# Kernel tuning notes

Measured on AMD Instinct MI355X. Metric: run time of the kernel, lower is better.

Reference implementation:

```python
import jax, jax.numpy as jnp
import numpy as np

TEMPERATURE = 0.1
LOSS_WEIGHT = 1.0


def setup_inputs() -> dict:
    key = jax.random.key(0)
    k1, k2 = jax.random.split(key)
    B, M, N, C = 8, 4096, 4096, 3
    pred_points = jax.random.normal(k1, (B, M, C), dtype=jnp.float32)
    gt_points = jax.random.normal(k2, (B, N, C), dtype=jnp.float32)
    return {"pred_points": pred_points, "gt_points": gt_points}


def _cdist(x, y):
    # Euclidean distance matrix [B, M, N] via the |x|^2 + |y|^2 - 2<x,y> identity
    x2 = jnp.sum(x * x, axis=-1)  # [B, M]
    y2 = jnp.sum(y * y, axis=-1)  # [B, N]
    xy = jnp.einsum('bmc,bnc->bmn', x, y)  # [B, M, N]
    d2 = x2[:, :, None] + y2[:, None, :] - 2.0 * xy
    return jnp.sqrt(jnp.maximum(d2, 0.0))


def reference(pred_points, gt_points):
    dists = _cdist(pred_points, gt_points)                # [B, M, N]
    soft_assign = jax.nn.softmax(-dists / TEMPERATURE, axis=2)  # softmin
    weighted = jnp.sum(soft_assign * dists, axis=2)       # [B, M]
    per_batch = jnp.mean(weighted, axis=1)                # [B]
    return jnp.mean(per_batch) * LOSS_WEIGHT              # scalar ('mean' reduction)
```

## Files before the change

### kernel.cpp

```cpp
#include <hip/hip_runtime.h>
#include <hip/hip_bf16.h>

#ifndef __has_builtin
#define __has_builtin(x) 0
#endif

#if __has_builtin(__builtin_amdgcn_exp2f)
#define FAST_EXP2(x) __builtin_amdgcn_exp2f(x)
#else
#define FAST_EXP2(x) exp2f(x)
#endif

#if __has_builtin(__builtin_amdgcn_sqrtf)
#define FAST_SQRT(x) __builtin_amdgcn_sqrtf(x)
#else
#define FAST_SQRT(x) sqrtf(x)
#endif

constexpr int kB = 8;
constexpr int kM = 4096;
constexpr int kN = 4096;
constexpr float C2  = 14.426950408889634f;
constexpr float C22 = C2 * C2;
#define POISON_U32 0xAAAAAAAAu

constexpr int RPL    = 4;
constexpr int ROWS   = 64 * RPL;
constexpr int WAVES  = 16;
constexpr int BLOCKT = 64 * WAVES;
constexpr int NROWG  = (kB * kM) / ROWS;
constexpr int    PART_OFF = 16;
constexpr size_t ws_need(int ns) { return (size_t)(PART_OFF + 2 * ns * kB * kM) * 4; }

template <int NSPLIT>
__global__ __launch_bounds__(BLOCKT, 8) void emd_partial_kernel(
    const float* __restrict__ pred, const float* __restrict__ gt,
    float* __restrict__ partL, float* __restrict__ partA) {
  constexpr int SEGN = kN / NSPLIT;
  constexpr int NPC  = SEGN / WAVES;
  __shared__ __align__(16) float4 g4[SEGN];
  __shared__ float red_l[WAVES][RPL][64];
  __shared__ float red_a[WAVES][RPL][64];

  const int tid  = threadIdx.x;
  const int lane = tid & 63;
  const int wv   = tid >> 6;
  const int rg   = blockIdx.x / NSPLIT;
  const int seg  = blockIdx.x % NSPLIT;
  const int rbase = rg * ROWS;
  const int b     = rbase >> 12;

  const float* gtb = gt + ((size_t)b * kN + (size_t)seg * SEGN) * 3;
  for (int i = tid; i < SEGN; i += BLOCKT) {
    const float* p = gtb + 3 * i;
    float x = p[0], y = p[1], z = p[2];
    g4[i] = make_float4(x, y, z, C22 * fmaf(x, x, fmaf(y, y, z * z)));
  }
  float nx[RPL], ny[RPL], nz[RPL], pq[RPL];
  const int m0 = (rbase & (kM - 1)) + lane;
#pragma unroll
  for (int r = 0; r < RPL; ++r) {
    const float* pp = pred + ((size_t)b * kM + m0 + r * 64) * 3;
    float x = pp[0], y = pp[1], z = pp[2];
    nx[r] = -2.0f * C22 * x;
    ny[r] = -2.0f * C22 * y;
    nz[r] = -2.0f * C22 * z;
    pq[r] = C22 * fmaf(x, x, fmaf(y, y, z * z));
  }
  __syncthreads();

  float l[RPL] = {};
  float a[RPL] = {};
  const int n0 = wv * NPC;
  for (int n = n0; n < n0 + NPC; n += 4) {
    float4 G[4];
#pragma unroll
    for (int j = 0; j < 4; ++j) G[j] = g4[n + j];
#pragma unroll
    for (int j = 0; j < 4; ++j) {
#pragma unroll
      for (int r = 0; r < RPL; ++r) {
        float s  = fmaf(nx[r], G[j].x,
                   fmaf(ny[r], G[j].y, fmaf(nz[r], G[j].z, G[j].w + pq[r])));
        float ds = FAST_SQRT(fmaxf(s, 0.0f));
        float p  = FAST_EXP2(-ds);
        l[r] += p;
        a[r] = fmaf(ds, p, a[r]);
      }
    }
  }
#pragma unroll
  for (int r = 0; r < RPL; ++r) {
    red_l[wv][r][lane] = l[r];
    red_a[wv][r][lane] = a[r];
  }
  __syncthreads();

  if (tid < 64 * RPL) {
    const int ln = tid & 63, r = tid >> 6;
    float lt = 0.f, at = 0.f;
#pragma unroll
    for (int c = 0; c < WAVES; ++c) { lt += red_l[c][r][ln]; at += red_a[c][r][ln]; }
    const int row = rbase + r * 64 + ln;
    partL[(size_t)seg * (kB * kM) + row] = lt;
    partA[(size_t)seg * (kB * kM) + row] = at;
  }
}

constexpr int CB      = 512;
constexpr int CBLOCKS = (kB * kM) / CB;
template <int NSEG>
__global__ __launch_bounds__(CB) void emd_combine_kernel(
    const float* __restrict__ partL, const float* __restrict__ partA,
    float* __restrict__ ws, float* __restrict__ out) {
  const int row = blockIdx.x * CB + threadIdx.x;
  float lt = 0.f, at = 0.f;
#pragma unroll
  for (int s = 0; s < NSEG; ++s) {
    lt += partL[(size_t)s * (kB * kM) + row];
    at += partA[(size_t)s * (kB * kM) + row];
  }
  float w = (at / lt) * (1.0f / (C2 * (float)(kB * kM)));
#pragma unroll
  for (int off = 32; off > 0; off >>= 1) w += __shfl_down(w, off, 64);
  __shared__ float sred[CB / 64];
  const int lane = threadIdx.x & 63, wv = threadIdx.x >> 6;
  if (lane == 0) sred[wv] = w;
  __syncthreads();
  if (threadIdx.x == 0) {
    float s = 0.f;
#pragma unroll
    for (int i = 0; i < CB / 64; ++i) s += sred[i];
    atomicAdd(&ws[0], s);
    __threadfence();
    unsigned t = atomicAdd((unsigned int*)(ws + 1), 1u);
    if (t == POISON_U32 + (unsigned)(CBLOCKS - 1)) {
      __threadfence();
      out[0] = atomicAdd(&ws[0], 0.0f);
    }
  }
}

constexpr int F_CHUNKS  = 16;
constexpr int F_BLOCKT  = 64 * F_CHUNKS;
constexpr int F_NPC     = kN / F_CHUNKS;
constexpr int F_NBLOCKS = (kB * kM) / 64;

__global__ __launch_bounds__(F_BLOCKT, 8) void emd_softmin_fallback(
    const float* __restrict__ pred, const float* __restrict__ gt,
    float* __restrict__ ws, float* __restrict__ out) {
  __shared__ __align__(16) float4 g4[kN];
  __shared__ float red_l[F_CHUNKS][64];
  __shared__ float red_a[F_CHUNKS][64];
  const int tid = threadIdx.x, lane = tid & 63, chunk = tid >> 6;
  const int rbase = blockIdx.x * 64;
  const int b = rbase >> 12;
  const int m = (rbase & (kM - 1)) + lane;
  const float* gtb = gt + (size_t)b * kN * 3;
  for (int i = tid; i < kN; i += F_BLOCKT) {
    const float* p = gtb + 3 * i;
    float x = p[0], y = p[1], z = p[2];
    g4[i] = make_float4(x, y, z, C22 * fmaf(x, x, fmaf(y, y, z * z)));
  }
  const float* pp_ptr = pred + ((size_t)b * kM + (size_t)m) * 3;
  const float px = pp_ptr[0], py = pp_ptr[1], pz = pp_ptr[2];
  const float nx = -2.0f * C22 * px, ny = -2.0f * C22 * py, nz = -2.0f * C22 * pz;
  const float pq = C22 * fmaf(px, px, fmaf(py, py, pz * pz));
  __syncthreads();
  float l0 = 0.f, l1 = 0.f, a0 = 0.f, a1 = 0.f;
  const int n0 = chunk * F_NPC;
#pragma unroll 2
  for (int n = n0; n < n0 + F_NPC; n += 2) {
    const float4 G0 = g4[n], G1 = g4[n + 1];
    {
      float s = fmaf(nx, G0.x, fmaf(ny, G0.y, fmaf(nz, G0.z, G0.w + pq)));
      float ds = FAST_SQRT(fmaxf(s, 0.f));
      float p = FAST_EXP2(-ds);
      l0 += p; a0 = fmaf(ds, p, a0);
    }
    {
      float s = fmaf(nx, G1.x, fmaf(ny, G1.y, fmaf(nz, G1.z, G1.w + pq)));
      float ds = FAST_SQRT(fmaxf(s, 0.f));
      float p = FAST_EXP2(-ds);
      l1 += p; a1 = fmaf(ds, p, a1);
    }
  }
  red_l[chunk][lane] = l0 + l1;
  red_a[chunk][lane] = a0 + a1;
  __syncthreads();
  if (tid < 64) {
    float lt = 0.f, at = 0.f;
#pragma unroll
    for (int c = 0; c < F_CHUNKS; ++c) { lt += red_l[c][tid]; at += red_a[c][tid]; }
    float w = (at / lt) * (1.0f / (C2 * (float)(kB * kM)));
#pragma unroll
    for (int off = 32; off > 0; off >>= 1) w += __shfl_down(w, off, 64);
    if (tid == 0) {
      atomicAdd(&ws[0], w);
      __threadfence();
      unsigned t = atomicAdd((unsigned int*)(ws + 1), 1u);
      if (t == POISON_U32 + (unsigned)(F_NBLOCKS - 1)) {
        __threadfence();
        out[0] = atomicAdd(&ws[0], 0.0f);
      }
    }
  }
}

extern "C" void kernel_launch(void* const* d_in, const int* in_sizes, int n_in,
                              void* d_out, int out_size, void* d_ws, size_t ws_size,
                              hipStream_t stream) {
  const float* pred = (const float*)d_in[0];
  const float* gt   = (const float*)d_in[1];
  float* out = (float*)d_out;
  float* ws  = (float*)d_ws;

  if (ws_size >= ws_need(4)) {
    float* partL = ws + PART_OFF;
    float* partA = partL + (size_t)4 * kB * kM;
    emd_partial_kernel<4><<<NROWG * 4, BLOCKT, 0, stream>>>(pred, gt, partL, partA);
    emd_combine_kernel<4><<<CBLOCKS, CB, 0, stream>>>(partL, partA, ws, out);
  } else if (ws_size >= ws_need(2)) {
    float* partL = ws + PART_OFF;
    float* partA = partL + (size_t)2 * kB * kM;
    emd_partial_kernel<2><<<NROWG * 2, BLOCKT, 0, stream>>>(pred, gt, partL, partA);
    emd_combine_kernel<2><<<CBLOCKS, CB, 0, stream>>>(partL, partA, ws, out);
  } else {
    emd_softmin_fallback<<<F_NBLOCKS, F_BLOCKT, 0, stream>>>(pred, gt, ws, out);
  }
}
```

Measured before the change: 94.99 us.

## Precompute gt float4 in a prep kernel and stream it via wave-uniform scalar loads

Adds a prep kernel that packs gt points plus their scaled squared norm into a float4 buffer in the workspace. The main partial kernel then reads these through a wave-uniform pointer so the loads can become scalar loads, with a one-iteration software prefetch, and drops the LDS staging and the barrier. This targets LDS read bandwidth and the per-block gt repacking. It costs an extra kernel launch, a larger workspace requirement, and reliance on the compiler actually emitting scalar loads. The old LDS kernels remain as fallbacks, and the launch-bounds occupancy hint drops from 8 to 4.

```diff
diff --git a/kernel.cpp b/kernel.cpp
--- a/kernel.cpp
+++ b/kernel.cpp
@@ -29,16 +29,25 @@
 constexpr int WAVES  = 16;
 constexpr int BLOCKT = 64 * WAVES;
 constexpr int NROWG  = (kB * kM) / ROWS;
-constexpr int    PART_OFF = 16;
-constexpr size_t ws_need(int ns) { return (size_t)(PART_OFF + 2 * ns * kB * kM) * 4; }
-
-template <int NSPLIT>
-__global__ __launch_bounds__(BLOCKT, 8) void emd_partial_kernel(
-    const float* __restrict__ pred, const float* __restrict__ gt,
+constexpr int NSPLIT = 4;
+constexpr int    PART_OFF  = 16;
+constexpr size_t GT4_FLOATS = (size_t)kB * kN * 4;
+constexpr size_t ws_need_old(int ns) { return (size_t)(PART_OFF + 2 * ns * kB * kM) * 4; }
+constexpr size_t WS_NEED_SGPR = (PART_OFF + GT4_FLOATS + (size_t)2 * NSPLIT * kB * kM) * 4;
+
+__global__ __launch_bounds__(256) void emd_prep_kernel(
+    const float* __restrict__ gt, float4* __restrict__ gt4) {
+  const int i = blockIdx.x * 256 + threadIdx.x;
+  const float* p = gt + 3 * (size_t)i;
+  float x = p[0], y = p[1], z = p[2];
+  gt4[i] = make_float4(x, y, z, C22 * fmaf(x, x, fmaf(y, y, z * z)));
+}
+
+__global__ __launch_bounds__(BLOCKT, 4) void emd_partial_sgpr(
+    const float* __restrict__ pred, const float4* __restrict__ gt4,
     float* __restrict__ partL, float* __restrict__ partA) {
   constexpr int SEGN = kN / NSPLIT;
   constexpr int NPC  = SEGN / WAVES;
-  __shared__ __align__(16) float4 g4[SEGN];
   __shared__ float red_l[WAVES][RPL][64];
   __shared__ float red_a[WAVES][RPL][64];
 
@@ -50,12 +59,6 @@
   const int rbase = rg * ROWS;
   const int b     = rbase >> 12;
 
-  const float* gtb = gt + ((size_t)b * kN + (size_t)seg * SEGN) * 3;
-  for (int i = tid; i < SEGN; i += BLOCKT) {
-    const float* p = gtb + 3 * i;
-    float x = p[0], y = p[1], z = p[2];
-    g4[i] = make_float4(x, y, z, C22 * fmaf(x, x, fmaf(y, y, z * z)));
-  }
   float nx[RPL], ny[RPL], nz[RPL], pq[RPL];
   const int m0 = (rbase & (kM - 1)) + lane;
 #pragma unroll
@@ -67,27 +70,36 @@
     nz[r] = -2.0f * C22 * z;
     pq[r] = C22 * fmaf(x, x, fmaf(y, y, z * z));
   }
-  __syncthreads();
+
+  const int wvu = __builtin_amdgcn_readfirstlane(wv);
+  const float4* __restrict__ gq =
+      gt4 + (size_t)b * kN + (size_t)seg * SEGN + (size_t)wvu * NPC;
 
   float l[RPL] = {};
   float a[RPL] = {};
-  const int n0 = wv * NPC;
-  for (int n = n0; n < n0 + NPC; n += 4) {
-    float4 G[4];
-#pragma unroll
-    for (int j = 0; j < 4; ++j) G[j] = g4[n + j];
-#pragma unroll
-    for (int j = 0; j < 4; ++j) {
-#pragma unroll
-      for (int r = 0; r < RPL; ++r) {
-        float s  = fmaf(nx[r], G[j].x,
-                   fmaf(ny[r], G[j].y, fmaf(nz[r], G[j].z, G[j].w + pq[r])));
-        float ds = FAST_SQRT(fmaxf(s, 0.0f));
-        float p  = FAST_EXP2(-ds);
-        l[r] += p;
-        a[r] = fmaf(ds, p, a[r]);
-      }
+  float4 c0 = gq[0], c1 = gq[1], c2 = gq[2], c3 = gq[3];
+  for (int k = 0; k < NPC; k += 4) {
+    const int kn = (k + 4 < NPC) ? k + 4 : 0;
+    float4 n0 = gq[kn], n1 = gq[kn + 1], n2 = gq[kn + 2], n3 = gq[kn + 3];
+#define BODY(G, r)                                                       \
+    {                                                                    \
+      float u  = fmaf(nx[r], G.x,                                        \
+                 fmaf(ny[r], G.y, fmaf(nz[r], G.z, G.w + pq[r])));       \
+      float ds = FAST_SQRT(fmaxf(u, 0.0f));                \
+      float p  = FAST_EXP2(-ds);                        \
+      l[r] += p;                                                         \
+      a[r] = fmaf(ds, p, a[r]);                                          \
     }
+#pragma unroll
+    for (int r = 0; r < RPL; ++r) BODY(c0, r)
+#pragma unroll
+    for (int r = 0; r < RPL; ++r) BODY(c1, r)
+#pragma unroll
+    for (int r = 0; r < RPL; ++r) BODY(c2, r)
+#pragma unroll
+    for (int r = 0; r < RPL; ++r) BODY(c3, r)
+#undef BODY
+    c0 = n0; c1 = n1; c2 = n2; c3 = n3;
   }
 #pragma unroll
   for (int r = 0; r < RPL; ++r) {
@@ -141,11 +153,67 @@
   }
 }
 
-constexpr int F_CHUNKS  = 16;
-constexpr int F_BLOCKT  = 64 * F_CHUNKS;
-constexpr int F_NPC     = kN / F_CHUNKS;
-constexpr int F_NBLOCKS = (kB * kM) / 64;
-
+template <int NS>
+__global__ __launch_bounds__(BLOCKT, 4) void emd_partial_lds(
+    const float* __restrict__ pred, const float* __restrict__ gt,
+    float* __restrict__ partL, float* __restrict__ partA) {
+  constexpr int SEGN = kN / NS;
+  constexpr int NPC  = SEGN / WAVES;
+  __shared__ __align__(16) float4 g4[SEGN];
+  __shared__ float red_l[WAVES][RPL][64];
+  __shared__ float red_a[WAVES][RPL][64];
+  const int tid = threadIdx.x, lane = tid & 63, wv = tid >> 6;
+  const int rg = blockIdx.x / NS, seg = blockIdx.x % NS;
+  const int rbase = rg * ROWS, b = rbase >> 12;
+  const float* gtb = gt + ((size_t)b * kN + (size_t)seg * SEGN) * 3;
+  for (int i = tid; i < SEGN; i += BLOCKT) {
+    const float* p = gtb + 3 * i;
+    float x = p[0], y = p[1], z = p[2];
+    g4[i] = make_float4(x, y, z, C22 * fmaf(x, x, fmaf(y, y, z * z)));
+  }
+  float nx[RPL], ny[RPL], nz[RPL], pq[RPL];
+  const int m0 = (rbase & (kM - 1)) + lane;
+#pragma unroll
+  for (int r = 0; r < RPL; ++r) {
+    const float* pp = pred + ((size_t)b * kM + m0 + r * 64) * 3;
+    float x = pp[0], y = pp[1], z = pp[2];
+    nx[r] = -2.0f * C22 * x; ny[r] = -2.0f * C22 * y; nz[r] = -2.0f * C22 * z;
+    pq[r] = C22 * fmaf(x, x, fmaf(y, y, z * z));
+  }
+  __syncthreads();
+  float l[RPL] = {}, a[RPL] = {};
+  const int n0 = wv * NPC;
+  for (int n = n0; n < n0 + NPC; n += 4) {
+    float4 G[4];
+#pragma unroll
+    for (int j = 0; j < 4; ++j) G[j] = g4[n + j];
+#pragma unroll
+    for (int j = 0; j < 4; ++j)
+#pragma unroll
+      for (int r = 0; r < RPL; ++r) {
+        float u  = fmaf(nx[r], G[j].x,
+                   fmaf(ny[r], G[j].y, fmaf(nz[r], G[j].z, G[j].w + pq[r])));
+        float ds = FAST_SQRT(fmaxf(u, 0.0f));
+        float p  = FAST_EXP2(-ds);
+        l[r] += p; a[r] = fmaf(ds, p, a[r]);
+      }
+  }
+#pragma unroll
+  for (int r = 0; r < RPL; ++r) { red_l[wv][r][lane] = l[r]; red_a[wv][r][lane] = a[r]; }
+  __syncthreads();
+  if (tid < 64 * RPL) {
+    const int ln = tid & 63, r = tid >> 6;
+    float lt = 0.f, at = 0.f;
+#pragma unroll
+    for (int c = 0; c < WAVES; ++c) { lt += red_l[c][r][ln]; at += red_a[c][r][ln]; }
+    const int row = rbase + r * 64 + ln;
+    partL[(size_t)seg * (kB * kM) + row] = lt;
+    partA[(size_t)seg * (kB * kM) + row] = at;
+  }
+}
+
+constexpr int F_CHUNKS = 16, F_BLOCKT = 64 * F_CHUNKS;
+constexpr int F_NPC = kN / F_CHUNKS, F_NBLOCKS = (kB * kM) / 64;
 __global__ __launch_bounds__(F_BLOCKT, 8) void emd_softmin_fallback(
     const float* __restrict__ pred, const float* __restrict__ gt,
     float* __restrict__ ws, float* __restrict__ out) {
@@ -153,17 +221,15 @@
   __shared__ float red_l[F_CHUNKS][64];
   __shared__ float red_a[F_CHUNKS][64];
   const int tid = threadIdx.x, lane = tid & 63, chunk = tid >> 6;
-  const int rbase = blockIdx.x * 64;
-  const int b = rbase >> 12;
-  const int m = (rbase & (kM - 1)) + lane;
+  const int rbase = blockIdx.x * 64, b = rbase >> 12, m = (rbase & (kM - 1)) + lane;
   const float* gtb = gt + (size_t)b * kN * 3;
   for (int i = tid; i < kN; i += F_BLOCKT) {
     const float* p = gtb + 3 * i;
     float x = p[0], y = p[1], z = p[2];
     g4[i] = make_float4(x, y, z, C22 * fmaf(x, x, fmaf(y, y, z * z)));
   }
-  const float* pp_ptr = pred + ((size_t)b * kM + (size_t)m) * 3;
-  const float px = pp_ptr[0], py = pp_ptr[1], pz = pp_ptr[2];
+  const float* pp = pred + ((size_t)b * kM + (size_t)m) * 3;
+  const float px = pp[0], py = pp[1], pz = pp[2];
   const float nx = -2.0f * C22 * px, ny = -2.0f * C22 * py, nz = -2.0f * C22 * pz;
   const float pq = C22 * fmaf(px, px, fmaf(py, py, pz * pz));
   __syncthreads();
@@ -172,21 +238,14 @@
 #pragma unroll 2
   for (int n = n0; n < n0 + F_NPC; n += 2) {
     const float4 G0 = g4[n], G1 = g4[n + 1];
-    {
-      float s = fmaf(nx, G0.x, fmaf(ny, G0.y, fmaf(nz, G0.z, G0.w + pq)));
-      float ds = FAST_SQRT(fmaxf(s, 0.f));
-      float p = FAST_EXP2(-ds);
-      l0 += p; a0 = fmaf(ds, p, a0);
-    }
-    {
-      float s = fmaf(nx, G1.x, fmaf(ny, G1.y, fmaf(nz, G1.z, G1.w + pq)));
-      float ds = FAST_SQRT(fmaxf(s, 0.f));
-      float p = FAST_EXP2(-ds);
-      l1 += p; a1 = fmaf(ds, p, a1);
-    }
-  }
-  red_l[chunk][lane] = l0 + l1;
-  red_a[chunk][lane] = a0 + a1;
+    { float u = fmaf(nx, G0.x, fmaf(ny, G0.y, fmaf(nz, G0.z, G0.w + pq)));
+      float ds = FAST_SQRT(fmaxf(u, 0.f)); float p = FAST_EXP2(-ds);
+      l0 += p; a0 = fmaf(ds, p, a0); }
+    { float u = fmaf(nx, G1.x, fmaf(ny, G1.y, fmaf(nz, G1.z, G1.w + pq)));
+      float ds = FAST_SQRT(fmaxf(u, 0.f)); float p = FAST_EXP2(-ds);
+      l1 += p; a1 = fmaf(ds, p, a1); }
+  }
+  red_l[chunk][lane] = l0 + l1; red_a[chunk][lane] = a0 + a1;
   __syncthreads();
   if (tid < 64) {
     float lt = 0.f, at = 0.f;
@@ -215,15 +274,22 @@
   float* out = (float*)d_out;
   float* ws  = (float*)d_ws;
 
-  if (ws_size >= ws_need(4)) {
+  if (ws_size >= WS_NEED_SGPR) {
+    float4* gt4  = (float4*)(ws + PART_OFF);
+    float* partL = ws + PART_OFF + GT4_FLOATS;
+    float* partA = partL + (size_t)NSPLIT * kB * kM;
+    emd_prep_kernel<<<(kB * kN) / 256, 256, 0, stream>>>(gt, gt4);
+    emd_partial_sgpr<<<NROWG * NSPLIT, BLOCKT, 0, stream>>>(pred, gt4, partL, partA);
+    emd_combine_kernel<NSPLIT><<<CBLOCKS, CB, 0, stream>>>(partL, partA, ws, out);
+  } else if (ws_size >= ws_need_old(4)) {
     float* partL = ws + PART_OFF;
     float* partA = partL + (size_t)4 * kB * kM;
-    emd_partial_kernel<4><<<NROWG * 4, BLOCKT, 0, stream>>>(pred, gt, partL, partA);
+    emd_partial_lds<4><<<NROWG * 4, BLOCKT, 0, stream>>>(pred, gt, partL, partA);
     emd_combine_kernel<4><<<CBLOCKS, CB, 0, stream>>>(partL, partA, ws, out);
-  } else if (ws_size >= ws_need(2)) {
+  } else if (ws_size >= ws_need_old(2)) {
     float* partL = ws + PART_OFF;
     float* partA = partL + (size_t)2 * kB * kM;
-    emd_partial_kernel<2><<<NROWG * 2, BLOCKT, 0, stream>>>(pred, gt, partL, partA);
+    emd_partial_lds<2><<<NROWG * 2, BLOCKT, 0, stream>>>(pred, gt, partL, partA);
     emd_combine_kernel<2><<<CBLOCKS, CB, 0, stream>>>(partL, partA, ws, out);
   } else {
     emd_softmin_fallback<<<F_NBLOCKS, F_BLOCKT, 0, stream>>>(pred, gt, ws, out);
```

Result: no change. 96.88 us (+2.0%).
